# Optimization experiments

Measured on AMD Instinct MI355X. Metric: run time of the kernel, lower is better.

The kernel has to match this reference:

```python
import jax, jax.numpy as jnp
import numpy as np

D = 2          # qudit dimension
L = 22         # number of qudits; state length = D**L = 4194304
INDEX = tuple(range(L))  # rotation applied on every qudit (angle[i] indexed by qudit position)

# Generator S = Sx(j=0, k=1) on a D-level system: |0><1| + |1><0|
def _make_S():
    S = np.zeros((D, D), dtype=np.complex64)
    S[0, 1] = 1.0
    S[1, 0] = 1.0
    return jnp.asarray(S)


def setup_inputs() -> dict:
    key = jax.random.key(0)
    k1, k2, k3 = jax.random.split(key, 3)
    n = D ** L
    x_real = jax.random.normal(k1, (n,), dtype=jnp.float32)
    x_imag = jax.random.normal(k2, (n,), dtype=jnp.float32)
    angle = jax.random.uniform(k3, (L,), dtype=jnp.float32)
    return {"x_real": x_real, "x_imag": x_imag, "angle": angle}


def reference(x_real, x_imag, angle):
    # U = kron_i expm(-0.5j * angle[i] * S)  (identity on qudits not in INDEX),
    # applied as U @ x. Instead of materializing the D^L x D^L sparse unitary,
    # apply each single-qudit gate by contracting axis i of the reshaped state,
    # which is exactly the same linear map.
    S = _make_S()
    psi = (x_real + 1j * x_imag).astype(jnp.complex64).reshape((D,) * L)
    for i in range(L):
        if i in INDEX:
            M = jax.scipy.linalg.expm((-0.5j) * angle[i].astype(jnp.complex64) * S)
            # contract qudit axis i: psi'[..., a, ...] = sum_b M[a,b] psi[..., b, ...]
            psi = jnp.moveaxis(jnp.tensordot(M, psi, axes=([1], [i])), 0, i)
        # else: identity, nothing to do
    out = psi.reshape(-1)
    return jnp.stack([out.real, out.imag])  # (2, D**L) float32
```

## Files before the change

### kernel.cpp

```cpp
#include <hip/hip_runtime.h>


constexpr int NTOT = 1 << 22;

__device__ __forceinline__ void rotg(float& ar, float& ai, float& br, float& bi,
                                     float c, float s) {
    float t0 = ar, t1 = ai, t2 = br, t3 = bi;
    ar = fmaf(c, t0,  s * t3);
    ai = fmaf(c, t1, -s * t2);
    br = fmaf(c, t2,  s * t1);
    bi = fmaf(c, t3, -s * t0);
}

template<int K0, int NB, int MSH>
__device__ __forceinline__ void gatesM(float (&ar)[16], float (&ai)[16],
                                       const float* __restrict__ ang) {
    #pragma unroll
    for (int b = 0; b < NB; ++b) {
        const int m = 1 << (MSH + b);
        const float a = 0.5f * ang[21 - (K0 + b)];
        const float c = cosf(a), s = sinf(a);
        #pragma unroll
        for (int j = 0; j < 16; ++j)
            if (!(j & m)) rotg(ar[j], ai[j], ar[j | m], ai[j | m], c, s);
    }
}

__device__ __forceinline__ int slotA(int i) { return i ^ ((i >> 4) & 15); }

__global__ __launch_bounds__(512, 4) void rgate_A(const float* __restrict__ xr,
                                                  const float* __restrict__ xi,
                                                  const float* __restrict__ ang,
                                                  float* __restrict__ out) {
    __shared__ float2 sv[8192];
    const int t  = threadIdx.x;
    const int g0 = blockIdx.x << 13;

    float ar[16], ai[16];
    #pragma unroll
    for (int q = 0; q < 4; ++q) {
        const int i = (t << 2) + (q << 11);
        float4 vr = *(const float4*)(xr + g0 + i);
        float4 vi = *(const float4*)(xi + g0 + i);
        ar[4*q+0] = vr.x; ar[4*q+1] = vr.y; ar[4*q+2] = vr.z; ar[4*q+3] = vr.w;
        ai[4*q+0] = vi.x; ai[4*q+1] = vi.y; ai[4*q+2] = vi.z; ai[4*q+3] = vi.w;
    }
    gatesM<11, 2, 2>(ar, ai, ang);

    #pragma unroll
    for (int q = 0; q < 4; ++q)
        #pragma unroll
        for (int r = 0; r < 4; ++r)
            sv[slotA((t << 2) + r + (q << 11))] = make_float2(ar[4*q+r], ai[4*q+r]);
    __syncthreads();

    const int b2 = (t & 3) + ((t >> 2) << 6);
    #pragma unroll
    for (int j = 0; j < 16; ++j) {
        float2 v = sv[slotA(b2 + (j << 2))];
        ar[j] = v.x; ai[j] = v.y;
    }
    gatesM<2, 4, 0>(ar, ai, ang);
    #pragma unroll
    for (int j = 0; j < 16; ++j)
        sv[slotA(b2 + (j << 2))] = make_float2(ar[j], ai[j]);
    __syncthreads();

    const int b3 = (t & 63) + ((t >> 6) << 10);
    #pragma unroll
    for (int j = 0; j < 16; ++j) {
        float2 v = sv[slotA(b3 + (j << 6))];
        ar[j] = v.x; ai[j] = v.y;
    }
    gatesM<6, 4, 0>(ar, ai, ang);
    #pragma unroll
    for (int j = 0; j < 16; ++j)
        sv[slotA(b3 + (j << 6))] = make_float2(ar[j], ai[j]);
    __syncthreads();

    const int b4 = ((t & 255) << 2) + ((t >> 8) << 12);
    #pragma unroll
    for (int q = 0; q < 4; ++q)
        #pragma unroll
        for (int r = 0; r < 4; ++r) {
            float2 v = sv[slotA(b4 + r + (q << 10))];
            ar[4*q+r] = v.x; ai[4*q+r] = v.y;
        }
    gatesM<0, 2, 0>(ar, ai, ang);
    gatesM<10, 1, 2>(ar, ai, ang);

    #pragma unroll
    for (int q = 0; q < 4; ++q) {
        const int i = b4 + (q << 10);
        *(float4*)(out + g0 + i)        = make_float4(ar[4*q], ar[4*q+1], ar[4*q+2], ar[4*q+3]);
        *(float4*)(out + NTOT + g0 + i) = make_float4(ai[4*q], ai[4*q+1], ai[4*q+2], ai[4*q+3]);
    }
}

__global__ __launch_bounds__(512, 4) void rgate_B(const float* __restrict__ ang,
                                                  float* __restrict__ out) {
    __shared__ float2 sv[8192];
    const int t   = threadIdx.x;
    const int bid = blockIdx.x;
    const int blk = (bid >> 3) | ((bid & 7) << 6);
    const int sub = t & 15, hw = t >> 4;
    const int lbase = (blk << 4) + sub;
    float* outr = out;
    float* outi = out + NTOT;

    float ar[16], ai[16];
    #pragma unroll
    for (int j = 0; j < 16; ++j) {
        const int g = ((j | (hw << 4)) << 13) + lbase;
        ar[j] = outr[g]; ai[j] = outi[g];
    }
    gatesM<13, 4, 0>(ar, ai, ang);

    {
        const float a = 0.5f * ang[21 - 17];
        const float c = cosf(a), s = sinf(a);
        #pragma unroll
        for (int j = 0; j < 16; ++j) {
            float pr = __shfl_xor(ar[j], 16, 64);
            float pi = __shfl_xor(ai[j], 16, 64);
            ar[j] = fmaf(c, ar[j],  s * pi);
            ai[j] = fmaf(c, ai[j], -s * pr);
        }
    }

    #pragma unroll
    for (int j = 0; j < 16; ++j)
        sv[((j | (hw << 4)) << 4) + sub] = make_float2(ar[j], ai[j]);
    __syncthreads();

    #pragma unroll
    for (int j = 0; j < 16; ++j) {
        float2 v = sv[((hw | (j << 5)) << 4) + sub];
        ar[j] = v.x; ai[j] = v.y;
    }
    gatesM<18, 4, 0>(ar, ai, ang);

    #pragma unroll
    for (int j = 0; j < 16; ++j) {
        const int g = ((hw | (j << 5)) << 13) + lbase;
        outr[g] = ar[j]; outi[g] = ai[j];
    }
}

extern "C" void kernel_launch(void* const* d_in, const int* in_sizes, int n_in,
                              void* d_out, int out_size, void* d_ws, size_t ws_size,
                              hipStream_t stream) {
    const float* xr  = (const float*)d_in[0];
    const float* xi  = (const float*)d_in[1];
    const float* ang = (const float*)d_in[2];
    float* out = (float*)d_out;

    rgate_A<<<512, 512, 0, stream>>>(xr, xi, ang, out);
    rgate_B<<<512, 512, 0, stream>>>(ang, out);
}
```

Before: 106.5 us.

## Split rotation gates into three passes with smaller blocks and vectorized strided access

Restructures the two-kernel gate application into three passes over 4096-element tiles. The first pass handles the low 12 qudits with shared memory and wave shuffles, and two strided passes handle qudits 12-16 and 17-21 using float2 accesses and float4 shared-memory transposes. It aims to improve coalescing and occupancy of the strided pass, but adds a full extra read/write sweep of the state.

```diff
diff --git a/kernel.cpp b/kernel.cpp
--- a/kernel.cpp
+++ b/kernel.cpp
@@ -26,125 +26,141 @@
     }
 }
 
-__device__ __forceinline__ int slotA(int i) { return i ^ ((i >> 4) & 15); }
+template<int XOR>
+__device__ __forceinline__ void shflgate(float (&ar)[16], float (&ai)[16],
+                                         float c, float s) {
+    #pragma unroll
+    for (int j = 0; j < 16; ++j) {
+        float pr = __shfl_xor(ar[j], XOR, 64);
+        float pi = __shfl_xor(ai[j], XOR, 64);
+        ar[j] = fmaf(c, ar[j],  s * pi);
+        ai[j] = fmaf(c, ai[j], -s * pr);
+    }
+}
 
-__global__ __launch_bounds__(512, 4) void rgate_A(const float* __restrict__ xr,
-                                                  const float* __restrict__ xi,
-                                                  const float* __restrict__ ang,
-                                                  float* __restrict__ out) {
-    __shared__ float2 sv[8192];
+__device__ __forceinline__ int swz(int i) { return i ^ (((i >> 6) & 15) << 2); }
+
+__global__ __launch_bounds__(256, 4) void rgate_p1(const float* __restrict__ xr,
+                                                   const float* __restrict__ xi,
+                                                   const float* __restrict__ ang,
+                                                   float* __restrict__ out) {
+    __shared__ float2 sv[4096];
     const int t  = threadIdx.x;
-    const int g0 = blockIdx.x << 13;
+    const int g0 = blockIdx.x << 12;
 
     float ar[16], ai[16];
     #pragma unroll
     for (int q = 0; q < 4; ++q) {
-        const int i = (t << 2) + (q << 11);
-        float4 vr = *(const float4*)(xr + g0 + i);
-        float4 vi = *(const float4*)(xi + g0 + i);
+        const int m = (t << 2) + (q << 10);
+        float4 vr = *(const float4*)(xr + g0 + m);
+        float4 vi = *(const float4*)(xi + g0 + m);
         ar[4*q+0] = vr.x; ar[4*q+1] = vr.y; ar[4*q+2] = vr.z; ar[4*q+3] = vr.w;
         ai[4*q+0] = vi.x; ai[4*q+1] = vi.y; ai[4*q+2] = vi.z; ai[4*q+3] = vi.w;
     }
-    gatesM<11, 2, 2>(ar, ai, ang);
+    gatesM<0, 2, 0>(ar, ai, ang);
+    gatesM<10, 2, 2>(ar, ai, ang);
 
     #pragma unroll
-    for (int q = 0; q < 4; ++q)
+    for (int q = 0; q < 4; ++q) {
+        const int m = swz((t << 2) + (q << 10));
         #pragma unroll
         for (int r = 0; r < 4; ++r)
-            sv[slotA((t << 2) + r + (q << 11))] = make_float2(ar[4*q+r], ai[4*q+r]);
+            sv[m + r] = make_float2(ar[4*q+r], ai[4*q+r]);
+    }
     __syncthreads();
 
-    const int b2 = (t & 3) + ((t >> 2) << 6);
+    const int b2 = (t & 3) | ((t >> 2) << 6);
     #pragma unroll
     for (int j = 0; j < 16; ++j) {
-        float2 v = sv[slotA(b2 + (j << 2))];
+        float2 v = sv[swz(b2 + (j << 2))];
         ar[j] = v.x; ai[j] = v.y;
     }
     gatesM<2, 4, 0>(ar, ai, ang);
     #pragma unroll
     for (int j = 0; j < 16; ++j)
-        sv[slotA(b2 + (j << 2))] = make_float2(ar[j], ai[j]);
+        sv[swz(b2 + (j << 2))] = make_float2(ar[j], ai[j]);
     __syncthreads();
 
-    const int b3 = (t & 63) + ((t >> 6) << 10);
+    const int b3 = ((t & 15) << 2) | ((t >> 4) << 8);
     #pragma unroll
-    for (int j = 0; j < 16; ++j) {
-        float2 v = sv[slotA(b3 + (j << 6))];
-        ar[j] = v.x; ai[j] = v.y;
-    }
-    gatesM<6, 4, 0>(ar, ai, ang);
-    #pragma unroll
-    for (int j = 0; j < 16; ++j)
-        sv[slotA(b3 + (j << 6))] = make_float2(ar[j], ai[j]);
-    __syncthreads();
-
-    const int b4 = ((t & 255) << 2) + ((t >> 8) << 12);
-    #pragma unroll
-    for (int q = 0; q < 4; ++q)
+    for (int jj = 0; jj < 4; ++jj) {
+        const int m = swz(b3 + (jj << 6));
         #pragma unroll
         for (int r = 0; r < 4; ++r) {
-            float2 v = sv[slotA(b4 + r + (q << 10))];
-            ar[4*q+r] = v.x; ai[4*q+r] = v.y;
+            float2 v = sv[m + r];
+            ar[4*jj+r] = v.x; ai[4*jj+r] = v.y;
         }
-    gatesM<0, 2, 0>(ar, ai, ang);
-    gatesM<10, 1, 2>(ar, ai, ang);
-
+    }
+    gatesM<6, 2, 2>(ar, ai, ang);
+    {
+        float a8 = 0.5f * ang[21 - 8], a9 = 0.5f * ang[21 - 9];
+        shflgate<16>(ar, ai, cosf(a8), sinf(a8));
+        shflgate<32>(ar, ai, cosf(a9), sinf(a9));
+    }
     #pragma unroll
-    for (int q = 0; q < 4; ++q) {
-        const int i = b4 + (q << 10);
-        *(float4*)(out + g0 + i)        = make_float4(ar[4*q], ar[4*q+1], ar[4*q+2], ar[4*q+3]);
-        *(float4*)(out + NTOT + g0 + i) = make_float4(ai[4*q], ai[4*q+1], ai[4*q+2], ai[4*q+3]);
+    for (int jj = 0; jj < 4; ++jj) {
+        const int m = b3 + (jj << 6);
+        *(float4*)(out + g0 + m)        = make_float4(ar[4*jj], ar[4*jj+1], ar[4*jj+2], ar[4*jj+3]);
+        *(float4*)(out + NTOT + g0 + m) = make_float4(ai[4*jj], ai[4*jj+1], ai[4*jj+2], ai[4*jj+3]);
     }
 }
 
-__global__ __launch_bounds__(512, 4) void rgate_B(const float* __restrict__ ang,
-                                                  float* __restrict__ out) {
-    __shared__ float2 sv[8192];
+template<int KBASE, int HSH>
+__device__ __forceinline__ void rgate_strided(const float* __restrict__ ang,
+                                              float* __restrict__ out,
+                                              int base) {
+    __shared__ float2 sv[4096];
     const int t   = threadIdx.x;
-    const int bid = blockIdx.x;
-    const int blk = (bid >> 3) | ((bid & 7) << 6);
-    const int sub = t & 15, hw = t >> 4;
-    const int lbase = (blk << 4) + sub;
+    const int sub = t & 63, hw = t >> 6;
     float* outr = out;
     float* outi = out + NTOT;
 
     float ar[16], ai[16];
     #pragma unroll
-    for (int j = 0; j < 16; ++j) {
-        const int g = ((j | (hw << 4)) << 13) + lbase;
-        ar[j] = outr[g]; ai[j] = outi[g];
+    for (int j = 0; j < 8; ++j) {
+        const int g = base + ((j | (hw << 3)) << HSH);
+        float2 vr = *(const float2*)(outr + g);
+        float2 vi = *(const float2*)(outi + g);
+        ar[2*j] = vr.x; ar[2*j+1] = vr.y;
+        ai[2*j] = vi.x; ai[2*j+1] = vi.y;
     }
-    gatesM<13, 4, 0>(ar, ai, ang);
-
-    {
-        const float a = 0.5f * ang[21 - 17];
-        const float c = cosf(a), s = sinf(a);
-        #pragma unroll
-        for (int j = 0; j < 16; ++j) {
-            float pr = __shfl_xor(ar[j], 16, 64);
-            float pi = __shfl_xor(ai[j], 16, 64);
-            ar[j] = fmaf(c, ar[j],  s * pi);
-            ai[j] = fmaf(c, ai[j], -s * pr);
-        }
-    }
+    gatesM<KBASE, 3, 1>(ar, ai, ang);
 
     #pragma unroll
-    for (int j = 0; j < 16; ++j)
-        sv[((j | (hw << 4)) << 4) + sub] = make_float2(ar[j], ai[j]);
+    for (int j = 0; j < 8; ++j) {
+        const int idx = ((j | (hw << 3)) << 7) + 2 * sub;
+        *(float4*)(&sv[idx]) = make_float4(ar[2*j], ai[2*j], ar[2*j+1], ai[2*j+1]);
+    }
     __syncthreads();
 
     #pragma unroll
-    for (int j = 0; j < 16; ++j) {
-        float2 v = sv[((hw | (j << 5)) << 4) + sub];
-        ar[j] = v.x; ai[j] = v.y;
+    for (int j = 0; j < 8; ++j) {
+        const int idx = ((hw | (j << 2)) << 7) + 2 * sub;
+        float4 v = *(const float4*)(&sv[idx]);
+        ar[2*j] = v.x; ai[2*j] = v.y;
+        ar[2*j+1] = v.z; ai[2*j+1] = v.w;
     }
-    gatesM<18, 4, 0>(ar, ai, ang);
+    gatesM<KBASE + 3, 2, 2>(ar, ai, ang);
 
     #pragma unroll
-    for (int j = 0; j < 16; ++j) {
-        const int g = ((hw | (j << 5)) << 13) + lbase;
-        outr[g] = ar[j]; outi[g] = ai[j];
+    for (int j = 0; j < 8; ++j) {
+        const int g = base + ((hw | (j << 2)) << HSH);
+        *(float2*)(outr + g) = make_float2(ar[2*j], ar[2*j+1]);
+        *(float2*)(outi + g) = make_float2(ai[2*j], ai[2*j+1]);
     }
+}
+
+__global__ __launch_bounds__(256, 4) void rgate_p2(const float* __restrict__ ang,
+                                                   float* __restrict__ out) {
+    const int u = blockIdx.x >> 5, c = blockIdx.x & 31;
+    const int base = (u << 17) + (c << 7) + 2 * (threadIdx.x & 63);
+    rgate_strided<12, 12>(ang, out, base);
+}
+
+__global__ __launch_bounds__(256, 4) void rgate_p3(const float* __restrict__ ang,
+                                                   float* __restrict__ out) {
+    const int base = (blockIdx.x << 7) + 2 * (threadIdx.x & 63);
+    rgate_strided<17, 17>(ang, out, base);
 }
 
 extern "C" void kernel_launch(void* const* d_in, const int* in_sizes, int n_in,
@@ -155,6 +171,7 @@
     const float* ang = (const float*)d_in[2];
     float* out = (float*)d_out;
 
-    rgate_A<<<512, 512, 0, stream>>>(xr, xi, ang, out);
-    rgate_B<<<512, 512, 0, stream>>>(ang, out);
+    rgate_p1<<<1024, 256, 0, stream>>>(xr, xi, ang, out);
+    rgate_p2<<<1024, 256, 0, stream>>>(ang, out);
+    rgate_p3<<<1024, 256, 0, stream>>>(ang, out);
 }
```

Result: slower. 114.0 us (+7.1%).

## Split gate application into three passes with smaller blocks and shuffle-based gates

Applied to the files above, without the earlier changes.

Restructures the two-kernel gate schedule into three kernels. The first handles the low 12 qubits in 4096-element blocks of 256 threads, replacing one block barrier with a wave-local LDS wait. Two register-only strided kernels then each apply five high-qubit gates, using a 32-lane shuffle for one of them, which removes the shared-memory transpose from the second kernel. This adds a third full read/write pass over the 32 MB state in exchange for fewer barriers and higher occupancy.

```diff
diff --git a/kernel.cpp b/kernel.cpp
--- a/kernel.cpp
+++ b/kernel.cpp
@@ -18,133 +18,113 @@
     #pragma unroll
     for (int b = 0; b < NB; ++b) {
         const int m = 1 << (MSH + b);
-        const float a = 0.5f * ang[21 - (K0 + b)];
-        const float c = cosf(a), s = sinf(a);
+        float c, s;
+        sincosf(0.5f * ang[21 - (K0 + b)], &s, &c);
         #pragma unroll
         for (int j = 0; j < 16; ++j)
             if (!(j & m)) rotg(ar[j], ai[j], ar[j | m], ai[j | m], c, s);
     }
 }
 
-__device__ __forceinline__ int slotA(int i) { return i ^ ((i >> 4) & 15); }
+template<int XOR>
+__device__ __forceinline__ void shflgate(float (&ar)[16], float (&ai)[16],
+                                         float c, float s) {
+    #pragma unroll
+    for (int j = 0; j < 16; ++j) {
+        float pr = __shfl_xor(ar[j], XOR, 64);
+        float pi = __shfl_xor(ai[j], XOR, 64);
+        ar[j] = fmaf(c, ar[j],  s * pi);
+        ai[j] = fmaf(c, ai[j], -s * pr);
+    }
+}
 
-__global__ __launch_bounds__(512, 4) void rgate_A(const float* __restrict__ xr,
-                                                  const float* __restrict__ xi,
-                                                  const float* __restrict__ ang,
-                                                  float* __restrict__ out) {
-    __shared__ float2 sv[8192];
-    const int t  = threadIdx.x;
-    const int g0 = blockIdx.x << 13;
+__device__ __forceinline__ int slot(int i) { return i ^ ((i >> 4) & 15); }
+
+__global__ __launch_bounds__(256) void rgate_A(const float* __restrict__ xr,
+                                               const float* __restrict__ xi,
+                                               const float* __restrict__ ang,
+                                               float* __restrict__ out) {
+    __shared__ float2 sv[4096];
+    const int t = threadIdx.x;
+    const int l = t & 63, w = t >> 6;
+    const int g0 = blockIdx.x << 12;
 
     float ar[16], ai[16];
     #pragma unroll
     for (int q = 0; q < 4; ++q) {
-        const int i = (t << 2) + (q << 11);
+        const int i = (w << 10) | (q << 8) | (l << 2);
         float4 vr = *(const float4*)(xr + g0 + i);
         float4 vi = *(const float4*)(xi + g0 + i);
         ar[4*q+0] = vr.x; ar[4*q+1] = vr.y; ar[4*q+2] = vr.z; ar[4*q+3] = vr.w;
         ai[4*q+0] = vi.x; ai[4*q+1] = vi.y; ai[4*q+2] = vi.z; ai[4*q+3] = vi.w;
     }
-    gatesM<11, 2, 2>(ar, ai, ang);
+    gatesM<0, 2, 0>(ar, ai, ang);
+    gatesM<8, 2, 2>(ar, ai, ang);
 
     #pragma unroll
     for (int q = 0; q < 4; ++q)
         #pragma unroll
         for (int r = 0; r < 4; ++r)
-            sv[slotA((t << 2) + r + (q << 11))] = make_float2(ar[4*q+r], ai[4*q+r]);
-    __syncthreads();
+            sv[slot((w << 10) | (q << 8) | (l << 2) | r)]
+                = make_float2(ar[4*q+r], ai[4*q+r]);
 
-    const int b2 = (t & 3) + ((t >> 2) << 6);
+    __asm__ volatile("s_waitcnt lgkmcnt(0)" ::: "memory");
+
+    const int b2 = (w << 10) | ((l >> 2) << 6) | (l & 3);
     #pragma unroll
     for (int j = 0; j < 16; ++j) {
-        float2 v = sv[slotA(b2 + (j << 2))];
+        float2 v = sv[slot(b2 | (j << 2))];
         ar[j] = v.x; ai[j] = v.y;
     }
     gatesM<2, 4, 0>(ar, ai, ang);
     #pragma unroll
     for (int j = 0; j < 16; ++j)
-        sv[slotA(b2 + (j << 2))] = make_float2(ar[j], ai[j]);
+        sv[slot(b2 | (j << 2))] = make_float2(ar[j], ai[j]);
     __syncthreads();
 
-    const int b3 = (t & 63) + ((t >> 6) << 10);
+    const int b3 = (w << 8) | l;
     #pragma unroll
     for (int j = 0; j < 16; ++j) {
-        float2 v = sv[slotA(b3 + (j << 6))];
+        float2 v = sv[slot(b3 | ((j & 3) << 6) | ((j >> 2) << 10))];
         ar[j] = v.x; ai[j] = v.y;
     }
-    gatesM<6, 4, 0>(ar, ai, ang);
-    #pragma unroll
-    for (int j = 0; j < 16; ++j)
-        sv[slotA(b3 + (j << 6))] = make_float2(ar[j], ai[j]);
-    __syncthreads();
-
-    const int b4 = ((t & 255) << 2) + ((t >> 8) << 12);
-    #pragma unroll
-    for (int q = 0; q < 4; ++q)
-        #pragma unroll
-        for (int r = 0; r < 4; ++r) {
-            float2 v = sv[slotA(b4 + r + (q << 10))];
-            ar[4*q+r] = v.x; ai[4*q+r] = v.y;
-        }
-    gatesM<0, 2, 0>(ar, ai, ang);
-    gatesM<10, 1, 2>(ar, ai, ang);
+    gatesM<6, 2, 0>(ar, ai, ang);
+    gatesM<10, 2, 2>(ar, ai, ang);
 
     #pragma unroll
-    for (int q = 0; q < 4; ++q) {
-        const int i = b4 + (q << 10);
-        *(float4*)(out + g0 + i)        = make_float4(ar[4*q], ar[4*q+1], ar[4*q+2], ar[4*q+3]);
-        *(float4*)(out + NTOT + g0 + i) = make_float4(ai[4*q], ai[4*q+1], ai[4*q+2], ai[4*q+3]);
+    for (int j = 0; j < 16; ++j) {
+        const int i = b3 | ((j & 3) << 6) | ((j >> 2) << 10);
+        out[g0 + i]        = ar[j];
+        out[NTOT + g0 + i] = ai[j];
     }
 }
 
-__global__ __launch_bounds__(512, 4) void rgate_B(const float* __restrict__ ang,
-                                                  float* __restrict__ out) {
-    __shared__ float2 sv[8192];
-    const int t   = threadIdx.x;
-    const int bid = blockIdx.x;
-    const int blk = (bid >> 3) | ((bid & 7) << 6);
-    const int sub = t & 15, hw = t >> 4;
-    const int lbase = (blk << 4) + sub;
+template<int KJ, int KU, int BL, int VS>
+__global__ __launch_bounds__(256) void rgate_s(const float* __restrict__ ang,
+                                               float* __restrict__ out) {
+    const int t = threadIdx.x, b = blockIdx.x;
+    const int base = (t & 31) | (((t >> 5) & 1) << KU) | ((t >> 6) << 5)
+                   | ((b & ((1 << BL) - 1)) << 7) | ((b >> BL) << VS);
     float* outr = out;
     float* outi = out + NTOT;
 
     float ar[16], ai[16];
     #pragma unroll
-    for (int j = 0; j < 16; ++j) {
-        const int g = ((j | (hw << 4)) << 13) + lbase;
-        ar[j] = outr[g]; ai[j] = outi[g];
-    }
-    gatesM<13, 4, 0>(ar, ai, ang);
+    for (int j = 0; j < 16; ++j) ar[j] = outr[base + (j << KJ)];
+    #pragma unroll
+    for (int j = 0; j < 16; ++j) ai[j] = outi[base + (j << KJ)];
 
+    gatesM<KJ, 4, 0>(ar, ai, ang);
     {
-        const float a = 0.5f * ang[21 - 17];
-        const float c = cosf(a), s = sinf(a);
-        #pragma unroll
-        for (int j = 0; j < 16; ++j) {
-            float pr = __shfl_xor(ar[j], 16, 64);
-            float pi = __shfl_xor(ai[j], 16, 64);
-            ar[j] = fmaf(c, ar[j],  s * pi);
-            ai[j] = fmaf(c, ai[j], -s * pr);
-        }
+        float c, s;
+        sincosf(0.5f * ang[21 - KU], &s, &c);
+        shflgate<32>(ar, ai, c, s);
     }
 
     #pragma unroll
-    for (int j = 0; j < 16; ++j)
-        sv[((j | (hw << 4)) << 4) + sub] = make_float2(ar[j], ai[j]);
-    __syncthreads();
-
+    for (int j = 0; j < 16; ++j) outr[base + (j << KJ)] = ar[j];
     #pragma unroll
-    for (int j = 0; j < 16; ++j) {
-        float2 v = sv[((hw | (j << 5)) << 4) + sub];
-        ar[j] = v.x; ai[j] = v.y;
-    }
-    gatesM<18, 4, 0>(ar, ai, ang);
-
-    #pragma unroll
-    for (int j = 0; j < 16; ++j) {
-        const int g = ((hw | (j << 5)) << 13) + lbase;
-        outr[g] = ar[j]; outi[g] = ai[j];
-    }
+    for (int j = 0; j < 16; ++j) outi[base + (j << KJ)] = ai[j];
 }
 
 extern "C" void kernel_launch(void* const* d_in, const int* in_sizes, int n_in,
@@ -155,6 +135,7 @@
     const float* ang = (const float*)d_in[2];
     float* out = (float*)d_out;
 
-    rgate_A<<<512, 512, 0, stream>>>(xr, xi, ang, out);
-    rgate_B<<<512, 512, 0, stream>>>(ang, out);
+    rgate_A<<<1024, 256, 0, stream>>>(xr, xi, ang, out);
+    rgate_s<12, 16, 5, 17><<<1024, 256, 0, stream>>>(ang, out);
+    rgate_s<17, 21, 10, 27><<<1024, 256, 0, stream>>>(ang, out);
 }
```

Measured after the change: 115.4 us. 1.08x slower.

## Replace shared-memory passes in rgate_A with wavefront shuffle gates

Applied to the files above, without the earlier changes.

Rewrites the bit assignment in rgate_A so qubits on lane bits are handled with cross-lane xor shuffles instead of two extra shared-memory round trips and syncthreads. The kernel now does a single LDS exchange, and the gate list is reordered to match. It also switches to sincosf and drops the occupancy hint from launch bounds. The cost is many more shuffle instructions (DPP/ds_swizzle or bpermute), and the shuffle form is not register-local, so the ALU work per element is the same or higher.

```diff
diff --git a/kernel.cpp b/kernel.cpp
--- a/kernel.cpp
+++ b/kernel.cpp
@@ -18,82 +18,89 @@
     #pragma unroll
     for (int b = 0; b < NB; ++b) {
         const int m = 1 << (MSH + b);
-        const float a = 0.5f * ang[21 - (K0 + b)];
-        const float c = cosf(a), s = sinf(a);
+        float c, s;
+        sincosf(0.5f * ang[21 - (K0 + b)], &s, &c);
         #pragma unroll
         for (int j = 0; j < 16; ++j)
             if (!(j & m)) rotg(ar[j], ai[j], ar[j | m], ai[j | m], c, s);
     }
 }
 
-__device__ __forceinline__ int slotA(int i) { return i ^ ((i >> 4) & 15); }
+template<int XOR>
+__device__ __forceinline__ void shflgate(float (&ar)[16], float (&ai)[16],
+                                         float c, float s) {
+    #pragma unroll
+    for (int j = 0; j < 16; ++j) {
+        float pr = __shfl_xor(ar[j], XOR, 64);
+        float pi = __shfl_xor(ai[j], XOR, 64);
+        ar[j] = fmaf(c, ar[j],  s * pi);
+        ai[j] = fmaf(c, ai[j], -s * pr);
+    }
+}
 
-__global__ __launch_bounds__(512, 4) void rgate_A(const float* __restrict__ xr,
-                                                  const float* __restrict__ xi,
-                                                  const float* __restrict__ ang,
-                                                  float* __restrict__ out) {
+__device__ __forceinline__ int slot(int i) { return i ^ ((i >> 4) & 15); }
+
+__global__ __launch_bounds__(512) void rgate_A(const float* __restrict__ xr,
+                                               const float* __restrict__ xi,
+                                               const float* __restrict__ ang,
+                                               float* __restrict__ out) {
     __shared__ float2 sv[8192];
-    const int t  = threadIdx.x;
+    const int t = threadIdx.x;
+    const int l = t & 63, w = t >> 6;
     const int g0 = blockIdx.x << 13;
+
+    const int base1 = (l << 2) | ((w & 3) << 8) | ((w >> 2) << 12);
 
     float ar[16], ai[16];
     #pragma unroll
     for (int q = 0; q < 4; ++q) {
-        const int i = (t << 2) + (q << 11);
+        const int i = base1 | (q << 10);
         float4 vr = *(const float4*)(xr + g0 + i);
         float4 vi = *(const float4*)(xi + g0 + i);
         ar[4*q+0] = vr.x; ar[4*q+1] = vr.y; ar[4*q+2] = vr.z; ar[4*q+3] = vr.w;
         ai[4*q+0] = vi.x; ai[4*q+1] = vi.y; ai[4*q+2] = vi.z; ai[4*q+3] = vi.w;
     }
-    gatesM<11, 2, 2>(ar, ai, ang);
+    gatesM<0, 2, 0>(ar, ai, ang);
+    gatesM<10, 2, 2>(ar, ai, ang);
+
+    {
+        float c, s;
+        sincosf(0.5f * ang[21 - 2], &s, &c); shflgate< 1>(ar, ai, c, s);
+        sincosf(0.5f * ang[21 - 3], &s, &c); shflgate< 2>(ar, ai, c, s);
+        sincosf(0.5f * ang[21 - 4], &s, &c); shflgate< 4>(ar, ai, c, s);
+        sincosf(0.5f * ang[21 - 5], &s, &c); shflgate< 8>(ar, ai, c, s);
+        sincosf(0.5f * ang[21 - 6], &s, &c); shflgate<16>(ar, ai, c, s);
+        sincosf(0.5f * ang[21 - 7], &s, &c); shflgate<32>(ar, ai, c, s);
+    }
 
     #pragma unroll
     for (int q = 0; q < 4; ++q)
         #pragma unroll
         for (int r = 0; r < 4; ++r)
-            sv[slotA((t << 2) + r + (q << 11))] = make_float2(ar[4*q+r], ai[4*q+r]);
+            sv[slot(base1 | (q << 10) | r)] = make_float2(ar[4*q+r], ai[4*q+r]);
     __syncthreads();
 
-    const int b2 = (t & 3) + ((t >> 2) << 6);
+    const int base2 = ((l & 15) << 2) | (((l >> 4) & 1) << 6) | ((w & 1) << 7)
+                    | ((w >> 1) << 10) | ((l >> 5) << 12);
     #pragma unroll
-    for (int j = 0; j < 16; ++j) {
-        float2 v = sv[slotA(b2 + (j << 2))];
-        ar[j] = v.x; ai[j] = v.y;
-    }
-    gatesM<2, 4, 0>(ar, ai, ang);
-    #pragma unroll
-    for (int j = 0; j < 16; ++j)
-        sv[slotA(b2 + (j << 2))] = make_float2(ar[j], ai[j]);
-    __syncthreads();
-
-    const int b3 = (t & 63) + ((t >> 6) << 10);
-    #pragma unroll
-    for (int j = 0; j < 16; ++j) {
-        float2 v = sv[slotA(b3 + (j << 6))];
-        ar[j] = v.x; ai[j] = v.y;
-    }
-    gatesM<6, 4, 0>(ar, ai, ang);
-    #pragma unroll
-    for (int j = 0; j < 16; ++j)
-        sv[slotA(b3 + (j << 6))] = make_float2(ar[j], ai[j]);
-    __syncthreads();
-
-    const int b4 = ((t & 255) << 2) + ((t >> 8) << 12);
-    #pragma unroll
-    for (int q = 0; q < 4; ++q)
+    for (int j = 0; j < 4; ++j)
         #pragma unroll
         for (int r = 0; r < 4; ++r) {
-            float2 v = sv[slotA(b4 + r + (q << 10))];
-            ar[4*q+r] = v.x; ai[4*q+r] = v.y;
+            float2 v = sv[slot(base2 | (j << 8) | r)];
+            ar[4*j+r] = v.x; ai[4*j+r] = v.y;
         }
-    gatesM<0, 2, 0>(ar, ai, ang);
-    gatesM<10, 1, 2>(ar, ai, ang);
+    gatesM<8, 2, 2>(ar, ai, ang);
+    {
+        float c, s;
+        sincosf(0.5f * ang[21 - 12], &s, &c);
+        shflgate<32>(ar, ai, c, s);
+    }
 
     #pragma unroll
-    for (int q = 0; q < 4; ++q) {
-        const int i = b4 + (q << 10);
-        *(float4*)(out + g0 + i)        = make_float4(ar[4*q], ar[4*q+1], ar[4*q+2], ar[4*q+3]);
-        *(float4*)(out + NTOT + g0 + i) = make_float4(ai[4*q], ai[4*q+1], ai[4*q+2], ai[4*q+3]);
+    for (int j = 0; j < 4; ++j) {
+        const int i = base2 | (j << 8);
+        *(float4*)(out + g0 + i)        = make_float4(ar[4*j], ar[4*j+1], ar[4*j+2], ar[4*j+3]);
+        *(float4*)(out + NTOT + g0 + i) = make_float4(ai[4*j], ai[4*j+1], ai[4*j+2], ai[4*j+3]);
     }
 }
 
@@ -117,15 +124,9 @@
     gatesM<13, 4, 0>(ar, ai, ang);
 
     {
-        const float a = 0.5f * ang[21 - 17];
-        const float c = cosf(a), s = sinf(a);
-        #pragma unroll
-        for (int j = 0; j < 16; ++j) {
-            float pr = __shfl_xor(ar[j], 16, 64);
-            float pi = __shfl_xor(ai[j], 16, 64);
-            ar[j] = fmaf(c, ar[j],  s * pi);
-            ai[j] = fmaf(c, ai[j], -s * pr);
-        }
+        float c, s;
+        sincosf(0.5f * ang[21 - 17], &s, &c);
+        shflgate<16>(ar, ai, c, s);
     }
 
     #pragma unroll
```

Result: slower. 109.9 us (+3.2%).
